# Performance work log

Hardware: AMD Instinct MI355X
Metric: run time of the kernel (lower is better)

## Reference

```python
import jax, jax.numpy as jnp
import numpy as np

B = 2048          # number of trees (batch)
K = 511           # nodes per complete binary tree (depth 9: levels 0..8)
DEPTH = 9
VOCAB = 200000
EDIM = 128


def setup_inputs() -> dict:
    key = jax.random.key(0)
    k1, k2, k3, k4 = jax.random.split(key, 4)
    N = B * K
    i = np.arange(K)
    lvl = np.floor(np.log2(i + 1)).astype(np.int32)            # level within tree, 0..8
    par_local = np.where(i > 0, (i - 1) // 2, 0).astype(np.int64)  # root points to itself
    offs = (np.arange(B, dtype=np.int64) * K)[:, None]
    parent = jnp.asarray((offs + par_local[None, :]).reshape(-1), dtype=jnp.int32)
    level = jnp.asarray(np.tile(lvl, B), dtype=jnp.int32)
    batch_id = jnp.asarray(np.repeat(np.arange(B, dtype=np.int64), K), dtype=jnp.int32)
    tokens = jax.random.randint(k1, (N,), 0, VOCAB, dtype=jnp.int32)
    emb_weight = jax.random.normal(k2, (VOCAB, EDIM), dtype=jnp.float32) * 0.02
    W = jax.random.normal(k3, (EDIM, EDIM), dtype=jnp.float32) * 0.05
    b = jax.random.normal(k4, (EDIM,), dtype=jnp.float32) * 0.01
    return {"emb_weight": emb_weight, "W": W, "b": b,
            "tokens": tokens, "parent": parent, "level": level, "batch_id": batch_id}


def reference(emb_weight, W, b, tokens, parent, level, batch_id):
    # per-node projection: W_c(embedding(token))  -> [N, EDIM]
    h = emb_weight[tokens] @ W + b
    # bottom-up child aggregation: h[parent] += h[child], deepest level first
    for l in range(DEPTH - 1, 0, -1):
        contrib = jnp.where((level == l)[:, None], h, 0.0)
        h = h.at[parent].add(contrib)
    # torch.max over all node_list snapshots == per-tree elementwise max of node
    # states, clamped at 0 by the zero rows of untouched batch_node snapshots.
    seg_max = jax.ops.segment_max(h, batch_id, num_segments=B)
    return jnp.maximum(seg_max, 0.0)
```

## Files before the change

kernel.cpp:

```cpp
#include <hip/hip_runtime.h>
#include <hip/hip_bf16.h>
#include <stdint.h>

#define VOCAB 200000
#define EDIM 128
#define NTREES 2048
#define KNODES 511
#define PROJ_GRID 1024

typedef __attribute__((ext_vector_type(4))) float f32x4;
typedef __attribute__((ext_vector_type(2))) float f32x2;
typedef __attribute__((ext_vector_type(8))) short s16x8;
typedef __attribute__((ext_vector_type(8))) unsigned short u16x8;

#define AS1 __attribute__((address_space(1)))
#define AS3 __attribute__((address_space(3)))

__device__ __forceinline__ unsigned short f2bf(float x) {
  unsigned u = __builtin_bit_cast(unsigned, x);
  return (unsigned short)((u + 0x7fffu + ((u >> 16) & 1u)) >> 16);
}
__device__ __forceinline__ float bf2f(unsigned short h) {
  unsigned u = ((unsigned)h) << 16;
  return __builtin_bit_cast(float, u);
}

__device__ __forceinline__ unsigned fp8enc(float v) {
  unsigned u = __builtin_bit_cast(unsigned, v);
  unsigned s = (u >> 24) & 0x80u;
  unsigned au = u & 0x7fffffffu;
  au = au > 0x43E00000u ? 0x43E00000u : au;
  unsigned r = au + 0x0007ffffu + ((au >> 20) & 1u);
  unsigned code = (((r >> 23) - 120u) << 3) | ((r >> 20) & 7u);
  float a = __builtin_bit_cast(float, au);
  unsigned sub = (unsigned)(int)rintf(a * 512.0f);
  unsigned c = (au < 0x3C800000u) ? sub : code;
  return c | s;
}
__device__ __forceinline__ float fp8dec(unsigned b) {
  unsigned e = (b >> 3) & 15u, m = b & 7u;
  float n = __builtin_bit_cast(float, ((e + 120u) << 23) | (m << 20));
  float sv = (float)(int)m * 0.001953125f;
  float v = e ? n : sv;
  return (b & 0x80u) ? -v : v;
}

__device__ __forceinline__ unsigned enc4(float a, float b, float c, float d) {
#if __has_builtin(__builtin_amdgcn_cvt_pk_fp8_f32)
  int pk = 0;
  pk = __builtin_amdgcn_cvt_pk_fp8_f32(a, b, pk, false);
  pk = __builtin_amdgcn_cvt_pk_fp8_f32(c, d, pk, true);
  return (unsigned)pk;
#else
  return fp8enc(a) | (fp8enc(b) << 8) | (fp8enc(c) << 16) | (fp8enc(d) << 24);
#endif
}

__device__ __forceinline__ void dec8(uint2 v, float* o) {
#if __has_builtin(__builtin_amdgcn_cvt_pk_f32_fp8)
  f32x2 a = __builtin_amdgcn_cvt_pk_f32_fp8(v.x, false);
  f32x2 b = __builtin_amdgcn_cvt_pk_f32_fp8(v.x, true);
  f32x2 c = __builtin_amdgcn_cvt_pk_f32_fp8(v.y, false);
  f32x2 d = __builtin_amdgcn_cvt_pk_f32_fp8(v.y, true);
  o[0] = a[0]; o[1] = a[1]; o[2] = b[0]; o[3] = b[1];
  o[4] = c[0]; o[5] = c[1]; o[6] = d[0]; o[7] = d[1];
#else
#pragma unroll
  for (int i = 0; i < 4; ++i) o[i] = fp8dec((v.x >> (8 * i)) & 0xFFu);
#pragma unroll
  for (int i = 0; i < 4; ++i) o[4 + i] = fp8dec((v.y >> (8 * i)) & 0xFFu);
#endif
}

__device__ __forceinline__ s16x8 cvt8(f32x4 a, f32x4 b) {
  u16x8 t;
#pragma unroll
  for (int i = 0; i < 4; ++i)
    t[i] = __builtin_bit_cast(unsigned short, __float2bfloat16(a[i]));
#pragma unroll
  for (int i = 0; i < 4; ++i)
    t[4 + i] = __builtin_bit_cast(unsigned short, __float2bfloat16(b[i]));
  return __builtin_bit_cast(s16x8, t);
}

__global__ __launch_bounds__(256) void wprep_kernel(
    const float* __restrict__ W, const float* __restrict__ b,
    unsigned short* __restrict__ WTb2, float* __restrict__ bsc) {
  int c = blockIdx.x * 256 + threadIdx.x;
  if (c < 2048) {
    int lane = c & 63, fr = c >> 6;
    int ks = fr >> 3, nt = fr & 7, q = lane >> 4, cl = lane & 15;
    u16x8 t;
#pragma unroll
    for (int j = 0; j < 8; ++j)
      t[j] = f2bf(W[(ks * 32 + q * 8 + j) * EDIM + nt * 16 + cl] * 64.0f);
    *(u16x8*)(WTb2 + c * 8) = t;
  }
  if (c < EDIM) bsc[c] = b[c] * 64.0f;
}

__global__ __launch_bounds__(256, 3) void proj_kernel(
    const float* __restrict__ emb, const unsigned short* __restrict__ WTb2,
    const float* __restrict__ bsc, unsigned char* __restrict__ T8) {
  __shared__ unsigned short WL[2048 * 8];
  __shared__ float LB[EDIM];

  const int tid = threadIdx.x;
  const int wv = tid >> 6, lane = tid & 63;
  const int q = lane >> 4, cl = lane & 15;

#pragma unroll
  for (int i = 0; i < 8; ++i) {
    const char* src = (const char*)WTb2 + wv * 8192 + i * 1024 + lane * 16;
    char* dst = (char*)WL + wv * 8192 + i * 1024;
    __builtin_amdgcn_global_load_lds((const AS1 unsigned int*)src,
                                     (AS3 unsigned int*)dst, 16, 0, 0);
  }
  if (tid < EDIM) LB[tid] = bsc[tid];
  __syncthreads();

  const int NTb = VOCAB / 64;

  int bt = blockIdx.x;
  const float* rp = emb + ((long)bt * 64 + wv * 16 + cl) * EDIM + q * 8;
  f32x4 ea[4], eb[4];
#pragma unroll
  for (int ks = 0; ks < 4; ++ks) {
    ea[ks] = *(const f32x4*)(rp + ks * 32);
    eb[ks] = *(const f32x4*)(rp + ks * 32 + 4);
  }

  for (;;) {
    const int btn = bt + PROJ_GRID;

    s16x8 ef[4];
#pragma unroll
    for (int ks = 0; ks < 4; ++ks) ef[ks] = cvt8(ea[ks], eb[ks]);

    if (btn < NTb) {
      const float* rpn = emb + ((long)btn * 64 + wv * 16 + cl) * EDIM + q * 8;
#pragma unroll
      for (int ks = 0; ks < 4; ++ks) {
        ea[ks] = *(const f32x4*)(rpn + ks * 32);
        eb[ks] = *(const f32x4*)(rpn + ks * 32 + 4);
      }
    }

    unsigned wo = 0;
    asm volatile("" : "+v"(wo));
    const char* wl = (const char*)WL + wo;
    const char* lb = (const char*)LB + wo;

    f32x4 acc[8];
#pragma unroll
    for (int nt = 0; nt < 8; ++nt) acc[nt] = (f32x4){0.f, 0.f, 0.f, 0.f};
#pragma unroll
    for (int ks = 0; ks < 4; ++ks) {
#pragma unroll
      for (int nt = 0; nt < 8; ++nt) {
        s16x8 wf = *(const s16x8*)(wl + (ks * 8 + nt) * 1024 + lane * 16);
        acc[nt] = __builtin_amdgcn_mfma_f32_16x16x32_bf16(wf, ef[ks], acc[nt], 0, 0, 0);
      }
    }

    const long row = (long)bt * 64 + wv * 16 + cl;
#pragma unroll
    for (int nt = 0; nt < 8; ++nt) {
      const int col0 = nt * 16 + q * 4;
      f32x4 bv = *(const f32x4*)(lb + col0 * 4);
      *(unsigned*)&T8[row * EDIM + col0] =
          enc4(acc[nt][0] + bv[0], acc[nt][1] + bv[1],
               acc[nt][2] + bv[2], acc[nt][3] + bv[3]);
    }

    if (btn >= NTb) break;
    bt = btn;
  }
}

__global__ __launch_bounds__(512, 4) void tree_kernel(
    const unsigned char* __restrict__ T8, const int* __restrict__ tokens,
    float* __restrict__ out) {
  __shared__ unsigned char P8[512][EDIM];
  unsigned char* lds = &P8[0][0];
  const int SOFF = 16384;
  const int MOFF = 53248;

  const int tid = threadIdx.x;
  const int tree = blockIdx.x;
  const int wv = tid >> 6, lane = tid & 63;

  const int* tk = tokens + (long)tree * KNODES;
  int toks[8];
#pragma unroll
  for (int i = 0; i < 8; ++i) {
    int node = wv * 64 + i * 8 + (lane >> 3);
    toks[i] = tk[node > 510 ? 510 : node];
  }
  const int chunk = (lane & 7) ^ ((lane >> 3) & 7);
#pragma unroll
  for (int i = 0; i < 8; ++i) {
    const unsigned char* src = T8 + (long)toks[i] * EDIM + chunk * 16;
    unsigned char* dst = &P8[wv * 64 + i * 8][0];
    __builtin_amdgcn_global_load_lds((const AS1 unsigned int*)src,
                                     (AS3 unsigned int*)dst, 16, 0, 0);
  }
  __syncthreads();

  auto ldP8 = [&](int row, int q8) -> uint2 {
    int g = q8 >> 1, h = q8 & 1;
    return *(const uint2*)(lds + row * 128 + (((g ^ (row & 7))) << 4) + h * 8);
  };
  auto saddr = [&](int slot, int q16) -> unsigned char* {
    return lds + SOFF + slot * 288 + ((q16 ^ (slot & 7)) << 4);
  };

  const int q = tid & 15;
  const int jg = tid >> 4;
  float rmax[8];
#pragma unroll
  for (int e = 0; e < 8; ++e) rmax[e] = 0.f;

  u16x8 sp7[4];
#pragma unroll
  for (int k = 0; k < 4; ++k) {
    const int p = jg + 32 * k, m = 127 + p;
    uint2 pr = ldP8(m, q);
    uint2 xr = ldP8(2 * m + 1, q);
    uint2 yr = ldP8(2 * m + 2, q);
    float pv[8], xv[8], yv[8];
    dec8(pr, pv); dec8(xr, xv); dec8(yr, yv);
#pragma unroll
    for (int e = 0; e < 8; ++e) {
      float sv = pv[e] + xv[e] + yv[e];
      rmax[e] = fmaxf(rmax[e], fmaxf(fmaxf(xv[e], yv[e]), sv));
      sp7[k][e] = f2bf(sv);
    }
  }
  __syncthreads();
#pragma unroll
  for (int k = 0; k < 4; ++k) *(u16x8*)saddr(jg + 32 * k, q) = sp7[k];
  __syncthreads();

  for (int l = 6; l >= 0; --l) {
    const int cnt = 1 << l;
    for (int p = jg; p < cnt; p += 32) {
      const int m = cnt - 1 + p;
      const int ps = p << (7 - l);
      const int c2s = ps + (1 << (6 - l));
      uint2 pr = ldP8(m, q);
      u16x8 c1 = *(const u16x8*)saddr(ps, q);
      u16x8 c2 = *(const u16x8*)saddr(c2s, q);
      float pv[8];
      dec8(pr, pv);
      u16x8 sp;
#pragma unroll
      for (int e = 0; e < 8; ++e) {
        float sv = pv[e] + bf2f(c1[e]) + bf2f(c2[e]);
        rmax[e] = fmaxf(rmax[e], sv);
        sp[e] = f2bf(sv);
      }
      *(u16x8*)saddr(ps, q) = sp;
    }
    __syncthreads();
  }

#pragma unroll
  for (int e = 0; e < 8; ++e) {
    rmax[e] = fmaxf(rmax[e], __shfl_xor(rmax[e], 16, 64));
    rmax[e] = fmaxf(rmax[e], __shfl_xor(rmax[e], 32, 64));
  }
  float* mb = (float*)(lds + MOFF);
  if (lane < 16) {
#pragma unroll
    for (int e = 0; e < 8; ++e) mb[wv * 128 + lane * 8 + e] = rmax[e];
  }
  __syncthreads();
  if (tid < 128) {
    float v = mb[tid];
#pragma unroll
    for (int w2 = 1; w2 < 8; ++w2) v = fmaxf(v, mb[w2 * 128 + tid]);
    out[(long)tree * 128 + tid] = v * 0.015625f;
  }
}

extern "C" void kernel_launch(void* const* d_in, const int* in_sizes, int n_in,
                              void* d_out, int out_size, void* d_ws, size_t ws_size,
                              hipStream_t stream) {
  const float* emb = (const float*)d_in[0];
  const float* W = (const float*)d_in[1];
  const float* b = (const float*)d_in[2];
  const int* tokens = (const int*)d_in[3];

  unsigned char* T8 = (unsigned char*)d_ws;
  unsigned short* WTb2 = (unsigned short*)((char*)d_ws + 25600000);
  float* bsc = (float*)((char*)d_ws + 25632768);
  float* out = (float*)d_out;

  wprep_kernel<<<8, 256, 0, stream>>>(W, b, WTb2, bsc);
  proj_kernel<<<PROJ_GRID, 256, 0, stream>>>(emb, WTb2, bsc, T8);
  tree_kernel<<<NTREES, 512, 0, stream>>>(T8, tokens, out);
}
```

Measured before the change: 67.51 us.

## Split projection into separate bf16 cast pass and non-persistent MFMA GEMM kernel

Replaces the persistent fused projection kernel, which read fp32 embeddings and converted them in registers, with two kernels. A standalone cast kernel writes a bf16 copy of the whole embedding table, and a one-shot GEMM kernel computes 128 rows per block, starting the accumulators from the bias. Results are staged through LDS so each row is written to the fp8 table with coalesced 16-byte stores. The split adds a full extra write and read of a 51 MB bf16 intermediate and one more launch, in exchange for simpler GEMM blocks and better store coalescing.

```diff
diff --git a/kernel.cpp b/kernel.cpp
--- a/kernel.cpp
+++ b/kernel.cpp
@@ -6,12 +6,12 @@
 #define EDIM 128
 #define NTREES 2048
 #define KNODES 511
-#define PROJ_GRID 1024
 
 typedef __attribute__((ext_vector_type(4))) float f32x4;
 typedef __attribute__((ext_vector_type(2))) float f32x2;
 typedef __attribute__((ext_vector_type(8))) short s16x8;
 typedef __attribute__((ext_vector_type(8))) unsigned short u16x8;
+typedef __attribute__((ext_vector_type(4))) unsigned int u32x4;
 
 #define AS1 __attribute__((address_space(1)))
 #define AS3 __attribute__((address_space(3)))
@@ -72,17 +72,6 @@
 #endif
 }
 
-__device__ __forceinline__ s16x8 cvt8(f32x4 a, f32x4 b) {
-  u16x8 t;
-#pragma unroll
-  for (int i = 0; i < 4; ++i)
-    t[i] = __builtin_bit_cast(unsigned short, __float2bfloat16(a[i]));
-#pragma unroll
-  for (int i = 0; i < 4; ++i)
-    t[4 + i] = __builtin_bit_cast(unsigned short, __float2bfloat16(b[i]));
-  return __builtin_bit_cast(s16x8, t);
-}
-
 __global__ __launch_bounds__(256) void wprep_kernel(
     const float* __restrict__ W, const float* __restrict__ b,
     unsigned short* __restrict__ WTb2, float* __restrict__ bsc) {
@@ -99,11 +88,37 @@
   if (c < EDIM) bsc[c] = b[c] * 64.0f;
 }
 
-__global__ __launch_bounds__(256, 3) void proj_kernel(
-    const float* __restrict__ emb, const unsigned short* __restrict__ WTb2,
+__global__ __launch_bounds__(256) void cast_kernel(
+    const float* __restrict__ src, unsigned short* __restrict__ dst) {
+  const long t = (long)blockIdx.x * 256 + threadIdx.x;
+  const long NCH = 3200000;
+  const long nthr = 3200L * 256;
+  long idx[4];
+  f32x4 a[4], b[4];
+#pragma unroll
+  for (int j = 0; j < 4; ++j) {
+    long c = t + j * nthr;
+    idx[j] = c < NCH ? c : (NCH - 1);
+    a[j] = *(const f32x4*)(src + idx[j] * 8);
+    b[j] = *(const f32x4*)(src + idx[j] * 8 + 4);
+  }
+#pragma unroll
+  for (int j = 0; j < 4; ++j) {
+    u16x8 o;
+#pragma unroll
+    for (int i = 0; i < 4; ++i) o[i] = f2bf(a[j][i]);
+#pragma unroll
+    for (int i = 0; i < 4; ++i) o[4 + i] = f2bf(b[j][i]);
+    *(u16x8*)(dst + idx[j] * 8) = o;
+  }
+}
+
+__global__ __launch_bounds__(256, 3) void gemm_kernel(
+    const unsigned short* __restrict__ Tbf, const unsigned short* __restrict__ WTb2,
     const float* __restrict__ bsc, unsigned char* __restrict__ T8) {
   __shared__ unsigned short WL[2048 * 8];
   __shared__ float LB[EDIM];
+  __shared__ char ST[4][32 * 144];
 
   const int tid = threadIdx.x;
   const int wv = tid >> 6, lane = tid & 63;
@@ -112,69 +127,66 @@
 #pragma unroll
   for (int i = 0; i < 8; ++i) {
     const char* src = (const char*)WTb2 + wv * 8192 + i * 1024 + lane * 16;
-    char* dst = (char*)WL + wv * 8192 + i * 1024;
+    char* dstp = (char*)WL + wv * 8192 + i * 1024;
     __builtin_amdgcn_global_load_lds((const AS1 unsigned int*)src,
-                                     (AS3 unsigned int*)dst, 16, 0, 0);
+                                     (AS3 unsigned int*)dstp, 16, 0, 0);
   }
   if (tid < EDIM) LB[tid] = bsc[tid];
-  __syncthreads();
-
-  const int NTb = VOCAB / 64;
-
-  int bt = blockIdx.x;
-  const float* rp = emb + ((long)bt * 64 + wv * 16 + cl) * EDIM + q * 8;
-  f32x4 ea[4], eb[4];
+
+  const long rowbase = (long)blockIdx.x * 128 + wv * 32;
+  long r0 = rowbase + cl, r1 = rowbase + 16 + cl;
+  if (r0 >= VOCAB) r0 = VOCAB - 1;
+  if (r1 >= VOCAB) r1 = VOCAB - 1;
+  s16x8 ef[2][4];
 #pragma unroll
   for (int ks = 0; ks < 4; ++ks) {
-    ea[ks] = *(const f32x4*)(rp + ks * 32);
-    eb[ks] = *(const f32x4*)(rp + ks * 32 + 4);
-  }
-
-  for (;;) {
-    const int btn = bt + PROJ_GRID;
-
-    s16x8 ef[4];
-#pragma unroll
-    for (int ks = 0; ks < 4; ++ks) ef[ks] = cvt8(ea[ks], eb[ks]);
-
-    if (btn < NTb) {
-      const float* rpn = emb + ((long)btn * 64 + wv * 16 + cl) * EDIM + q * 8;
-#pragma unroll
-      for (int ks = 0; ks < 4; ++ks) {
-        ea[ks] = *(const f32x4*)(rpn + ks * 32);
-        eb[ks] = *(const f32x4*)(rpn + ks * 32 + 4);
-      }
-    }
-
-    unsigned wo = 0;
-    asm volatile("" : "+v"(wo));
-    const char* wl = (const char*)WL + wo;
-    const char* lb = (const char*)LB + wo;
-
-    f32x4 acc[8];
-#pragma unroll
-    for (int nt = 0; nt < 8; ++nt) acc[nt] = (f32x4){0.f, 0.f, 0.f, 0.f};
-#pragma unroll
-    for (int ks = 0; ks < 4; ++ks) {
-#pragma unroll
-      for (int nt = 0; nt < 8; ++nt) {
-        s16x8 wf = *(const s16x8*)(wl + (ks * 8 + nt) * 1024 + lane * 16);
-        acc[nt] = __builtin_amdgcn_mfma_f32_16x16x32_bf16(wf, ef[ks], acc[nt], 0, 0, 0);
-      }
-    }
-
-    const long row = (long)bt * 64 + wv * 16 + cl;
+    ef[0][ks] = *(const s16x8*)(Tbf + r0 * EDIM + ks * 32 + q * 8);
+    ef[1][ks] = *(const s16x8*)(Tbf + r1 * EDIM + ks * 32 + q * 8);
+  }
+#pragma unroll
+  for (int rt = 0; rt < 2; ++rt)
+#pragma unroll
+    for (int ks = 0; ks < 4; ++ks) asm volatile("" : "+v"(ef[rt][ks]));
+
+  __syncthreads();
+
+  f32x4 acc[2][8];
+#pragma unroll
+  for (int nt = 0; nt < 8; ++nt) {
+    f32x4 bv = *(const f32x4*)(LB + nt * 16 + q * 4);
+    acc[0][nt] = bv;
+    acc[1][nt] = bv;
+  }
+#pragma unroll
+  for (int ks = 0; ks < 4; ++ks) {
 #pragma unroll
     for (int nt = 0; nt < 8; ++nt) {
-      const int col0 = nt * 16 + q * 4;
-      f32x4 bv = *(const f32x4*)(lb + col0 * 4);
-      *(unsigned*)&T8[row * EDIM + col0] =
-          enc4(acc[nt][0] + bv[0], acc[nt][1] + bv[1],
-               acc[nt][2] + bv[2], acc[nt][3] + bv[3]);
-    }
-
-    if (btn >= NTb) break;
-    bt = btn;
+      s16x8 wf = *(const s16x8*)((const char*)WL + (ks * 8 + nt) * 1024 + lane * 16);
+      acc[0][nt] = __builtin_amdgcn_mfma_f32_16x16x32_bf16(wf, ef[0][ks], acc[0][nt], 0, 0, 0);
+      acc[1][nt] = __builtin_amdgcn_mfma_f32_16x16x32_bf16(wf, ef[1][ks], acc[1][nt], 0, 0, 0);
+    }
+  }
+
+  char* sw = &ST[wv][0];
+#pragma unroll
+  for (int rt = 0; rt < 2; ++rt)
+#pragma unroll
+    for (int nt = 0; nt < 8; ++nt) {
+      unsigned pk = enc4(acc[rt][nt][0], acc[rt][nt][1], acc[rt][nt][2], acc[rt][nt][3]);
+      *(unsigned*)(sw + (rt * 16 + cl) * 144 + (nt * 4 + q) * 4) = pk;
+    }
+  asm volatile("s_waitcnt lgkmcnt(0)" ::: "memory");
+  __builtin_amdgcn_sched_barrier(0);
+
+#pragma unroll
+  for (int j = 0; j < 4; ++j) {
+    const int slot = j * 64 + lane;
+    const int rr = slot >> 3, c16 = slot & 7;
+    const long grow = rowbase + rr;
+    if (grow < VOCAB) {
+      u32x4 v = *(const u32x4*)(sw + rr * 144 + c16 * 16);
+      *(u32x4*)&T8[grow * EDIM + c16 * 16] = v;
+    }
   }
 }
 
@@ -293,11 +305,13 @@
   const int* tokens = (const int*)d_in[3];
 
   unsigned char* T8 = (unsigned char*)d_ws;
-  unsigned short* WTb2 = (unsigned short*)((char*)d_ws + 25600000);
-  float* bsc = (float*)((char*)d_ws + 25632768);
+  unsigned short* Tbf = (unsigned short*)((char*)d_ws + (32 << 20));
+  unsigned short* WTb2 = (unsigned short*)((char*)d_ws + (96 << 20));
+  float* bsc = (float*)((char*)d_ws + (96 << 20) + 32768);
   float* out = (float*)d_out;
 
   wprep_kernel<<<8, 256, 0, stream>>>(W, b, WTb2, bsc);
-  proj_kernel<<<PROJ_GRID, 256, 0, stream>>>(emb, WTb2, bsc, T8);
+  cast_kernel<<<3200, 256, 0, stream>>>(emb, Tbf);
+  gemm_kernel<<<1563, 256, 0, stream>>>(Tbf, WTb2, bsc, T8);
   tree_kernel<<<NTREES, 512, 0, stream>>>(T8, tokens, out);
 }
```

Measured after the change: 79.28 us. 1.17x slower.
